# Kernel optimization log

Hardware: AMD Instinct MI355X
Metric: run time of the kernel (lower is better)

The kernel has to match this reference:

```python
import jax, jax.numpy as jnp
import numpy as np

B, WIN, DM, DG, K = 32, 128, 1024, 64, 15  # batch, win_size(node feat dim), d_model(#nodes), graph embed, top_k


def setup_inputs() -> dict:
    key = jax.random.key(0)
    ks = jax.random.split(key, 7)
    sc_in = 1.0 / np.sqrt(WIN)
    return {
        "x": jax.random.normal(ks[0], (B, WIN, DM), jnp.float32),
        "Wq": jax.random.normal(ks[1], (DG, WIN), jnp.float32) * sc_in,
        "bq": jax.random.normal(ks[2], (DG,), jnp.float32) * 0.02,
        "Wk": jax.random.normal(ks[3], (DG, WIN), jnp.float32) * sc_in,
        "bk": jax.random.normal(ks[4], (DG,), jnp.float32) * 0.02,
        "Wg": jax.random.normal(ks[5], (WIN, WIN), jnp.float32) * sc_in,  # GCNConv lin weight [out,in]
        "bg": jax.random.normal(ks[6], (WIN,), jnp.float32) * 0.02,
    }


def _gcn_one(nf, Wq, bq, Wk, bk, Wg, bg):
    # nf: [N, F] node features (N = d_model, F = win_size)
    N = nf.shape[0]
    q = nf @ Wq.T + bq                      # [N, DG]
    k = nf @ Wk.T + bk                      # [N, DG]
    scores = (q @ k.T) * (1.0 / np.sqrt(DG))  # [N, N]
    scores = jnp.where(jnp.eye(N, dtype=bool), -jnp.inf, scores)
    _, tgt = jax.lax.top_k(scores, K)       # [N, K] top-k neighbors per source node
    src = jnp.repeat(jnp.arange(N), K)      # [N*K]
    tgt = tgt.reshape(-1)                   # [N*K]
    loops = jnp.arange(N)
    # manual self loops (module) + self loops added internally by GCNConv (default add_self_loops=True)
    src_all = jnp.concatenate([src, loops, loops])
    tgt_all = jnp.concatenate([tgt, loops, loops])
    # gcn_norm: degree over target (col) with unit edge weights
    deg = jax.ops.segment_sum(jnp.ones_like(tgt_all, jnp.float32), tgt_all, num_segments=N)
    dinv = jnp.where(deg > 0, jax.lax.rsqrt(deg), 0.0)
    norm = dinv[src_all] * dinv[tgt_all]    # [E]
    h = nf @ Wg.T                           # [N, F] linear transform (no bias inside lin)
    msg = h[src_all] * norm[:, None]        # gather + scale
    out = jax.ops.segment_sum(msg, tgt_all, num_segments=N) + bg  # scatter-add + bias
    return out                              # [N, F]


def reference(x, Wq, bq, Wk, bk, Wg, bg):
    # x: [B, win_size, d_model] -> nodes: [B, d_model, win_size]
    nodes = x.transpose(0, 2, 1)
    h = jax.vmap(lambda nf: _gcn_one(nf, Wq, bq, Wk, bk, Wg, bg))(nodes)  # [B, N, F]
    # n_layers == 1: no ReLU/dropout applied after last layer
    return h.transpose(0, 2, 1)  # [B, win_size, d_model]
```

## Files before the change

### kernel.cpp

```cpp
#include <hip/hip_runtime.h>

#define NBATCH 32
#define NN     1024
#define NF     128
#define NDG    64
#define TOPK   15

#define OFF_QH    ((size_t)0)
#define OFF_QL    ((size_t)4194304)
#define OFF_KH    ((size_t)8388608)
#define OFF_KL    ((size_t)12582912)
#define OFF_H     ((size_t)16777216)
#define OFF_DEG   ((size_t)33554432)
#define OFF_BMP   ((size_t)33685504)
#define OFF_WL    ((size_t)37879808)
#define OFF_TOPK  ((size_t)38010880)
#define OFF_W64   ((size_t)40108032)
#define OFF_QT64  ((size_t)40239104)
#define OFF_KT64  ((size_t)57016320)
#define OFF_TMP   ((size_t)0)

typedef short s8v  __attribute__((ext_vector_type(8)));
typedef float f4v  __attribute__((ext_vector_type(4)));
typedef unsigned short us8v __attribute__((ext_vector_type(8)));

__device__ inline unsigned short bf16_rne(float f) {
    unsigned u = __float_as_uint(f);
    return (unsigned short)((u + 0x7FFFu + ((u >> 16) & 1u)) >> 16);
}
__device__ inline float bf16_tof(unsigned short h) { return __uint_as_float(((unsigned)h) << 16); }

__device__ inline unsigned pack22(float s) {
    unsigned u   = __float_as_uint(s);
    int      mag = (int)(u & 0x7FFFFFFFu);
    int      t   = mag - 0x38800000;
    t = t < 0 ? 0 : (t > 0x07FFFFFF ? 0x07FFFFFF : t);
    unsigned ts = (unsigned)t >> 6;
    return ((int)u < 0) ? (0x1FFFFFu - ts) : (0x200000u | ts);
}
__device__ inline float dec22(unsigned val22) {
    bool pos = (val22 & 0x200000u) != 0;
    unsigned ts = pos ? (val22 & 0x1FFFFFu) : (0x1FFFFFu - (val22 & 0x1FFFFFu));
    float f = __uint_as_float((ts << 6) + 0x38800000u);
    return pos ? f : -f;
}

__global__ __launch_bounds__(256) void k_upcast(const float* __restrict__ Wq,
                                                const float* __restrict__ Wk,
                                                double* __restrict__ Wq64,
                                                double* __restrict__ Wk64) {
    int i = blockIdx.x * 256 + threadIdx.x;
    Wq64[i] = (double)Wq[i];
    Wk64[i] = (double)Wk[i];
}

__global__ __launch_bounds__(256) void k_prep(
    const float* __restrict__ x, const float* __restrict__ bq, const float* __restrict__ bk,
    const double* __restrict__ Wq64, const double* __restrict__ Wk64,
    const float* __restrict__ Wg,
    unsigned short* __restrict__ qh, unsigned short* __restrict__ ql,
    unsigned short* __restrict__ kh, unsigned short* __restrict__ kl,
    double* __restrict__ qT64, double* __restrict__ kT64,
    float* __restrict__ h,
    uint4* __restrict__ zbase, int zn)
{
    __shared__ float xs[64 * 129];
    const int t = threadIdx.x;
    const int l = t & 63;
    const int w = t >> 6;
    const int uw = __builtin_amdgcn_readfirstlane(w);
    const int n0 = blockIdx.x * 64;
    const int half = blockIdx.y;
    const int b  = blockIdx.z;

    {
        int lid = ((b * 2 + half) * 16 + blockIdx.x) * 256 + t;
        for (int i = lid; i < zn; i += 262144)
            zbase[i] = make_uint4(0u, 0u, 0u, 0u);
    }

    {
        const int j = t & 63, fg = t >> 6;
        for (int ff = 0; ff < 32; ++ff) {
            int f = fg + ff * 4;
            xs[j * 129 + f] = x[((size_t)b * NF + f) * NN + n0 + j];
        }
    }
    __syncthreads();

    {
        const int d0 = half * 32 + uw * 8;
        double accq[8], acck[8];
        #pragma unroll
        for (int dd = 0; dd < 8; ++dd) {
            accq[dd] = (double)bq[d0 + dd];
            acck[dd] = (double)bk[d0 + dd];
        }
        for (int fc = 0; fc < 32; ++fc) {
            double dx0 = (double)xs[l * 129 + fc * 4 + 0];
            double dx1 = (double)xs[l * 129 + fc * 4 + 1];
            double dx2 = (double)xs[l * 129 + fc * 4 + 2];
            double dx3 = (double)xs[l * 129 + fc * 4 + 3];
            #pragma unroll
            for (int dd = 0; dd < 8; ++dd) {
                int d = d0 + dd;
                const double* wq = &Wq64[d * NF + fc * 4];
                const double* wk = &Wk64[d * NF + fc * 4];
                accq[dd] += dx0 * wq[0] + dx1 * wq[1] + dx2 * wq[2] + dx3 * wq[3];
                acck[dd] += dx0 * wk[0] + dx1 * wk[1] + dx2 * wk[2] + dx3 * wk[3];
            }
        }
        #pragma unroll
        for (int dd = 0; dd < 8; ++dd) {
            size_t idx = ((size_t)b * NDG + d0 + dd) * NN + n0 + l;
            qT64[idx] = accq[dd];
            kT64[idx] = acck[dd];
        }
        us8v qh0, ql0, kh0, kl0;
        #pragma unroll
        for (int dd = 0; dd < 8; ++dd) {
            float fq = (float)accq[dd];
            unsigned short h1 = bf16_rne(fq);
            unsigned short l1 = bf16_rne(fq - bf16_tof(h1));
            float fk = (float)acck[dd];
            unsigned short h2 = bf16_rne(fk);
            unsigned short l2 = bf16_rne(fk - bf16_tof(h2));
            qh0[dd] = h1; ql0[dd] = l1; kh0[dd] = h2; kl0[dd] = l2;
        }
        size_t nb = ((size_t)b * NN + n0 + l) * NDG + d0;
        *(us8v*)&qh[nb] = qh0;
        *(us8v*)&ql[nb] = ql0;
        *(us8v*)&kh[nb] = kh0;
        *(us8v*)&kl[nb] = kl0;
    }

    {
        const int fp0 = half * 64 + uw * 16;
        float acc[16];
        #pragma unroll
        for (int i = 0; i < 16; ++i) acc[i] = 0.f;
        for (int fc = 0; fc < 32; ++fc) {
            float x0 = xs[l * 129 + fc * 4 + 0];
            float x1 = xs[l * 129 + fc * 4 + 1];
            float x2 = xs[l * 129 + fc * 4 + 2];
            float x3 = xs[l * 129 + fc * 4 + 3];
            #pragma unroll
            for (int ff = 0; ff < 16; ++ff) {
                const float* wg = &Wg[(fp0 + ff) * NF + fc * 4];
                acc[ff] += x0 * wg[0] + x1 * wg[1] + x2 * wg[2] + x3 * wg[3];
            }
        }
        __syncthreads();
        #pragma unroll
        for (int ff = 0; ff < 16; ++ff) xs[l * 129 + fp0 + ff] = acc[ff];
        __syncthreads();
        for (int r = 0; r < 16; ++r) {
            int idx = t + 256 * r;
            int n = idx >> 6, f = idx & 63;
            h[((size_t)b * NN + n0 + n) * NF + half * 64 + f] = xs[n * 129 + half * 64 + f];
        }
    }
}

#define CE(x,y) { unsigned a_ = v[x], b_ = v[y]; v[x] = a_ > b_ ? a_ : b_; v[y] = a_ > b_ ? b_ : a_; }
__device__ inline void sort16(unsigned v[16]) {
    CE(0,1) CE(2,3) CE(4,5) CE(6,7) CE(8,9) CE(10,11) CE(12,13) CE(14,15)
    CE(0,2) CE(1,3) CE(4,6) CE(5,7) CE(8,10) CE(9,11) CE(12,14) CE(13,15)
    CE(1,2) CE(5,6) CE(9,10) CE(13,14)
    CE(0,4) CE(1,5) CE(2,6) CE(3,7) CE(8,12) CE(9,13) CE(10,14) CE(11,15)
    CE(2,4) CE(3,5) CE(10,12) CE(11,13)
    CE(1,2) CE(3,4) CE(5,6) CE(9,10) CE(11,12) CE(13,14)
    CE(0,8) CE(1,9) CE(2,10) CE(3,11) CE(4,12) CE(5,13) CE(6,14) CE(7,15)
    CE(4,8) CE(5,9) CE(6,10) CE(7,11)
    CE(2,4) CE(3,5) CE(6,8) CE(7,9) CE(10,12) CE(11,13)
    CE(1,2) CE(3,4) CE(5,6) CE(7,8) CE(9,10) CE(11,12) CE(13,14)
}
__device__ inline void clean16(unsigned v[16]) {
    CE(0,8) CE(1,9) CE(2,10) CE(3,11) CE(4,12) CE(5,13) CE(6,14) CE(7,15)
    CE(0,4) CE(1,5) CE(2,6) CE(3,7) CE(8,12) CE(9,13) CE(10,14) CE(11,15)
    CE(0,2) CE(1,3) CE(4,6) CE(5,7) CE(8,10) CE(9,11) CE(12,14) CE(13,15)
    CE(0,1) CE(2,3) CE(4,5) CE(6,7) CE(8,9) CE(10,11) CE(12,13) CE(14,15)
}

__global__ __launch_bounds__(512, 4) void k_score(
    const unsigned short* __restrict__ qh, const unsigned short* __restrict__ ql,
    const unsigned short* __restrict__ kh, const unsigned short* __restrict__ kl,
    int* __restrict__ deg, unsigned int* __restrict__ bmp,
    int* __restrict__ topk, int* __restrict__ wl_cnt, int* __restrict__ wl)
{
    __shared__ unsigned short pkh[16 * 1024];
    __shared__ unsigned char  pkl[16 * 1024];
    const int t = threadIdx.x, l = t & 63, w = t >> 6;
    const int b = blockIdx.y, row0 = blockIdx.x * 16;
    const int m = l & 15, q4 = l >> 4;

    size_t abase = ((size_t)b * NN + row0 + m) * NDG + q4 * 8;
    s8v ah0 = *(const s8v*)&qh[abase];
    s8v ah1 = *(const s8v*)&qh[abase + 32];
    s8v al0 = *(const s8v*)&ql[abase];
    s8v al1 = *(const s8v*)&ql[abase + 32];

    const int colbase = w * 128;
    #pragma unroll
    for (int tt = 0; tt < 8; ++tt) {
        int col = colbase + tt * 16 + m;
        size_t bbase = ((size_t)b * NN + col) * NDG + q4 * 8;
        s8v bh0 = *(const s8v*)&kh[bbase];
        s8v bh1 = *(const s8v*)&kh[bbase + 32];
        s8v bl0 = *(const s8v*)&kl[bbase];
        s8v bl1 = *(const s8v*)&kl[bbase + 32];
        f4v acc = {0.f, 0.f, 0.f, 0.f};
        acc = __builtin_amdgcn_mfma_f32_16x16x32_bf16(al0, bl0, acc, 0, 0, 0);
        acc = __builtin_amdgcn_mfma_f32_16x16x32_bf16(al1, bl1, acc, 0, 0, 0);
        acc = __builtin_amdgcn_mfma_f32_16x16x32_bf16(ah0, bl0, acc, 0, 0, 0);
        acc = __builtin_amdgcn_mfma_f32_16x16x32_bf16(ah1, bl1, acc, 0, 0, 0);
        acc = __builtin_amdgcn_mfma_f32_16x16x32_bf16(al0, bh0, acc, 0, 0, 0);
        acc = __builtin_amdgcn_mfma_f32_16x16x32_bf16(al1, bh1, acc, 0, 0, 0);
        acc = __builtin_amdgcn_mfma_f32_16x16x32_bf16(ah0, bh0, acc, 0, 0, 0);
        acc = __builtin_amdgcn_mfma_f32_16x16x32_bf16(ah1, bh1, acc, 0, 0, 0);
        #pragma unroll
        for (int r = 0; r < 4; ++r) {
            int row  = q4 * 4 + r;
            int grow = row0 + row;
            float s = acc[r] * 0.125f;
            unsigned c22 = (col == grow) ? 0u : pack22(s);
            int pos = row * 1024 + (col ^ (q4 << 4));
            pkh[pos] = (unsigned short)(c22 >> 6);
            pkl[pos] = (unsigned char)(c22 & 63u);
        }
    }
    __syncthreads();

    for (int rr = 0; rr < 2; ++rr) {
        const int row = 2 * w + rr, grow = row0 + row;
        const int swz = (row >> 2) << 4;
        unsigned v[16];
        #pragma unroll
        for (int j = 0; j < 16; ++j) {
            int idx = row * 1024 + ((l + 64 * j) ^ swz);
            unsigned c22 = ((unsigned)pkh[idx] << 6) | (unsigned)pkl[idx];
            v[j] = (c22 << 10) | (unsigned)(1023 - (l + 64 * j));
        }
        sort16(v);
        #pragma unroll
        for (int off = 1; off < 64; off <<= 1) {
            unsigned pv[16];
            #pragma unroll
            for (int i = 0; i < 16; ++i) pv[i] = (unsigned)__shfl_xor((int)v[i], off, 64);
            #pragma unroll
            for (int i = 0; i < 8; ++i) {
                unsigned a0 = v[i], b0 = pv[15 - i];
                unsigned a1 = v[15 - i], b1 = pv[i];
                v[i]      = a0 > b0 ? a0 : b0;
                v[15 - i] = a1 > b1 ? a1 : b1;
            }
            clean16(v);
        }
        float s15 = dec22(v[14] >> 10), s16 = dec22(v[15] >> 10);
        unsigned e15 = (__float_as_uint(fabsf(s15)) >> 23) & 255u;
        unsigned e16 = (__float_as_uint(fabsf(s16)) >> 23) & 255u;
        unsigned e = e15 > e16 ? e15 : e16;
        float qq = __uint_as_float((e - 17) << 23);
        bool flagged = (s15 - s16) < (4.f * qq + 1e-4f);
        if (l < 15) {
            int col = 1023 - (int)(v[l] & 1023u);
            atomicAdd(&deg[b * NN + col], 1);
            atomicOr(&bmp[((size_t)b * NN + col) * 32 + (grow >> 5)], 1u << (grow & 31));
            if (flagged) topk[(b * NN + grow) * 16 + l] = col;
        }
        if (l == 0 && flagged) {
            int idx = atomicAdd(wl_cnt, 1);
            if (idx < 32767) wl[idx] = b * NN + grow;
        }
    }
}

__global__ __launch_bounds__(64) void k_repair(
    const double* __restrict__ qT64, const double* __restrict__ kT64,
    const int* __restrict__ topk, const int* __restrict__ wl_cnt, const int* __restrict__ wl,
    int* __restrict__ deg, unsigned int* __restrict__ bmp)
{
    const int l = threadIdx.x;
    __shared__ double qld[64];
    __shared__ int oldset[15], newset[15];
    const double NEGINF = -__builtin_inf();
    int n = wl_cnt[0]; if (n > 32767) n = 32767;

    for (int i = blockIdx.x; i < n; i += 1024) {
        int rg = wl[i];
        int b = rg >> 10, row = rg & 1023;

        __syncthreads();
        qld[l] = qT64[((size_t)b * NDG + l) * NN + row];
        if (l < 15) oldset[l] = topk[(b * NN + row) * 16 + l];
        __syncthreads();

        double sc[16];
        #pragma unroll
        for (int tt = 0; tt < 16; ++tt) sc[tt] = 0.0;
        const double* kb = &kT64[(size_t)b * NDG * NN];
        double buf[16];
        #pragma unroll
        for (int tt = 0; tt < 16; ++tt) buf[tt] = kb[l + 64 * tt];
        for (int d = 0; d < 64; ++d) {
            double nb[16];
            if (d < 63) {
                const double* kr = kb + (size_t)(d + 1) * NN;
                #pragma unroll
                for (int tt = 0; tt < 16; ++tt) nb[tt] = kr[l + 64 * tt];
            }
            double qd = qld[d];
            #pragma unroll
            for (int tt = 0; tt < 16; ++tt) sc[tt] += qd * buf[tt];
            if (d < 63) {
                #pragma unroll
                for (int tt = 0; tt < 16; ++tt) buf[tt] = nb[tt];
            }
        }
        #pragma unroll
        for (int tt = 0; tt < 16; ++tt) if (l + 64 * tt == row) sc[tt] = NEGINF;

        for (int it = 0; it < 15; ++it) {
            double lv = NEGINF; int lc = 0x7fffffff;
            #pragma unroll
            for (int tt = 0; tt < 16; ++tt)
                if (sc[tt] > lv) { lv = sc[tt]; lc = l + 64 * tt; }
            #pragma unroll
            for (int off = 1; off < 64; off <<= 1) {
                double ov = __shfl_xor(lv, off, 64);
                int    oc = __shfl_xor(lc, off, 64);
                if (ov > lv || (ov == lv && oc < lc)) { lv = ov; lc = oc; }
            }
            #pragma unroll
            for (int tt = 0; tt < 16; ++tt) if (l + 64 * tt == lc) sc[tt] = NEGINF;
            if (l == 0) newset[it] = lc;
        }
        __syncthreads();
        if (l < 15) {
            int cn = newset[l];
            bool found = false;
            #pragma unroll
            for (int j = 0; j < 15; ++j) found = found || (oldset[j] == cn);
            if (!found) {
                atomicAdd(&deg[b * NN + cn], 1);
                atomicOr(&bmp[((size_t)b * NN + cn) * 32 + (row >> 5)], 1u << (row & 31));
            }
            int co = oldset[l];
            found = false;
            #pragma unroll
            for (int j = 0; j < 15; ++j) found = found || (newset[j] == co);
            if (!found) {
                atomicSub(&deg[b * NN + co], 1);
                atomicAnd(&bmp[((size_t)b * NN + co) * 32 + (row >> 5)], ~(1u << (row & 31)));
            }
        }
    }
}

__global__ __launch_bounds__(128) void k_gather(
    const float* __restrict__ h, const float* __restrict__ bg,
    const int* __restrict__ deg, const unsigned int* __restrict__ bmp,
    float* __restrict__ tmp)
{
    __shared__ int list[1024];
    __shared__ float nrm[1024];
    __shared__ int scnt;
    const int tgt = blockIdx.x, b = blockIdx.y, t = threadIdx.x;
    if (t < 32) {
        unsigned word = bmp[((size_t)b * NN + tgt) * 32 + t];
        int pc = __popc(word);
        int pre = pc;
        #pragma unroll
        for (int d = 1; d < 32; d <<= 1) {
            int o = __shfl_up(pre, d, 32);
            if (t >= d) pre += o;
        }
        if (t == 31) scnt = pre;
        int idx = pre - pc;
        while (word) {
            int s = __ffs(word) - 1;
            word &= word - 1;
            list[idx++] = t * 32 + s;
        }
    }
    __syncthreads();
    const int cnt = scnt;
    for (int e = t; e < cnt; e += 128)
        nrm[e] = rsqrtf((float)(deg[b * NN + list[e]] + 2));
    __syncthreads();
    const int f = t;
    float dt = rsqrtf((float)(deg[b * NN + tgt] + 2));
    float acc = 2.0f * dt * h[((size_t)b * NN + tgt) * NF + f];
    for (int e = 0; e < cnt; ++e) {
        int src = list[e];
        acc += h[((size_t)b * NN + src) * NF + f] * nrm[e];
    }
    tmp[((size_t)b * NN + tgt) * NF + f] = bg[f] + dt * acc;
}

__global__ __launch_bounds__(256) void k_transpose(const float* __restrict__ tmp,
                                                   float* __restrict__ out)
{
    __shared__ float tile[32][33];
    const int t = threadIdx.x;
    const int n0 = blockIdx.x * 32, f0 = blockIdx.y * 32, b = blockIdx.z;
    const int c = t & 31, rb = t >> 5;
    #pragma unroll
    for (int i = 0; i < 4; ++i) {
        int r = rb + i * 8;
        tile[r][c] = tmp[((size_t)b * NN + n0 + r) * NF + f0 + c];
    }
    __syncthreads();
    #pragma unroll
    for (int i = 0; i < 4; ++i) {
        int r = rb + i * 8;
        out[((size_t)b * NF + f0 + r) * NN + n0 + c] = tile[c][r];
    }
}

extern "C" void kernel_launch(void* const* d_in, const int* in_sizes, int n_in,
                              void* d_out, int out_size, void* d_ws, size_t ws_size,
                              hipStream_t stream)
{
    const float* x  = (const float*)d_in[0];
    const float* Wq = (const float*)d_in[1];
    const float* bq = (const float*)d_in[2];
    const float* Wk = (const float*)d_in[3];
    const float* bk = (const float*)d_in[4];
    const float* Wg = (const float*)d_in[5];
    const float* bg = (const float*)d_in[6];
    float* out = (float*)d_out;
    char* ws = (char*)d_ws;

    unsigned short* qh = (unsigned short*)(ws + OFF_QH);
    unsigned short* ql = (unsigned short*)(ws + OFF_QL);
    unsigned short* kh = (unsigned short*)(ws + OFF_KH);
    unsigned short* kl = (unsigned short*)(ws + OFF_KL);
    float*          h   = (float*)(ws + OFF_H);
    int*            deg = (int*)(ws + OFF_DEG);
    unsigned int*   bmp = (unsigned int*)(ws + OFF_BMP);
    int*            wlc = (int*)(ws + OFF_WL);
    int*            wl  = wlc + 1;
    int*            tpk = (int*)(ws + OFF_TOPK);
    double*         Wq64 = (double*)(ws + OFF_W64);
    double*         Wk64 = Wq64 + 8192;
    double*         qT64 = (double*)(ws + OFF_QT64);
    double*         kT64 = (double*)(ws + OFF_KT64);
    float*          tmp  = (float*)(ws + OFF_TMP);

    k_upcast<<<32, 256, 0, stream>>>(Wq, Wk, Wq64, Wk64);
    k_prep<<<dim3(16, 2, 32), 256, 0, stream>>>(x, bq, bk, Wq64, Wk64, Wg,
                                                qh, ql, kh, kl, qT64, kT64, h,
                                                (uint4*)(ws + OFF_DEG), 270337);
    k_score<<<dim3(64, 32), 512, 0, stream>>>(qh, ql, kh, kl, deg, bmp, tpk, wlc, wl);
    k_repair<<<1024, 64, 0, stream>>>(qT64, kT64, tpk, wlc, wl, deg, bmp);
    k_gather<<<dim3(1024, 32), 128, 0, stream>>>(h, bg, deg, bmp, tmp);
    k_transpose<<<dim3(32, 4, 32), 256, 0, stream>>>(tmp, out);
}
```

Before: 311.6 us.

## Replace full wave bitonic top-k with threshold-filtered candidate selection

Each lane now takes the max of its 16 scores, and a 64-wide bitonic sort of those maxes gives the 16th-largest lane max as a threshold. Only elements at or above the threshold are compacted through shared memory and sorted once with a single 64-element bitonic sort. The full 1024-element merge sort stays as a fallback when more than 64 candidates survive. Scores are now stored as one packed 32-bit key (score plus column) instead of split short and byte arrays. This grows shared memory from 48KB to 64KB per block, which may lower occupancy.

```diff
diff --git a/kernel.cpp b/kernel.cpp
--- a/kernel.cpp
+++ b/kernel.cpp
@@ -182,14 +182,28 @@
     CE(0,1) CE(2,3) CE(4,5) CE(6,7) CE(8,9) CE(10,11) CE(12,13) CE(14,15)
 }
 
+__device__ inline unsigned bsort64(unsigned v, int l) {
+    #pragma unroll
+    for (int k = 2; k <= 64; k <<= 1) {
+        #pragma unroll
+        for (int j = k >> 1; j >= 1; j >>= 1) {
+            unsigned pv = (unsigned)__shfl_xor((int)v, j, 64);
+            bool tm = ((l & k) == 0) == ((l & j) == 0);
+            unsigned hi = v > pv ? v : pv;
+            unsigned lo = v > pv ? pv : v;
+            v = tm ? hi : lo;
+        }
+    }
+    return v;
+}
+
 __global__ __launch_bounds__(512, 4) void k_score(
     const unsigned short* __restrict__ qh, const unsigned short* __restrict__ ql,
     const unsigned short* __restrict__ kh, const unsigned short* __restrict__ kl,
     int* __restrict__ deg, unsigned int* __restrict__ bmp,
     int* __restrict__ topk, int* __restrict__ wl_cnt, int* __restrict__ wl)
 {
-    __shared__ unsigned short pkh[16 * 1024];
-    __shared__ unsigned char  pkl[16 * 1024];
+    __shared__ unsigned pk[16 * 1024];
     const int t = threadIdx.x, l = t & 63, w = t >> 6;
     const int b = blockIdx.y, row0 = blockIdx.x * 16;
     const int m = l & 15, q4 = l >> 4;
@@ -224,46 +238,77 @@
             int grow = row0 + row;
             float s = acc[r] * 0.125f;
             unsigned c22 = (col == grow) ? 0u : pack22(s);
-            int pos = row * 1024 + (col ^ (q4 << 4));
-            pkh[pos] = (unsigned short)(c22 >> 6);
-            pkl[pos] = (unsigned char)(c22 & 63u);
+            pk[row * 1024 + (col ^ (q4 << 4))] = (c22 << 10) | (unsigned)(1023 - col);
         }
     }
     __syncthreads();
 
     for (int rr = 0; rr < 2; ++rr) {
         const int row = 2 * w + rr, grow = row0 + row;
-        const int swz = (row >> 2) << 4;
         unsigned v[16];
         #pragma unroll
-        for (int j = 0; j < 16; ++j) {
-            int idx = row * 1024 + ((l + 64 * j) ^ swz);
-            unsigned c22 = ((unsigned)pkh[idx] << 6) | (unsigned)pkl[idx];
-            v[j] = (c22 << 10) | (unsigned)(1023 - (l + 64 * j));
-        }
-        sort16(v);
-        #pragma unroll
-        for (int off = 1; off < 64; off <<= 1) {
-            unsigned pv[16];
-            #pragma unroll
-            for (int i = 0; i < 16; ++i) pv[i] = (unsigned)__shfl_xor((int)v[i], off, 64);
-            #pragma unroll
-            for (int i = 0; i < 8; ++i) {
-                unsigned a0 = v[i], b0 = pv[15 - i];
-                unsigned a1 = v[15 - i], b1 = pv[i];
-                v[i]      = a0 > b0 ? a0 : b0;
-                v[15 - i] = a1 > b1 ? a1 : b1;
-            }
-            clean16(v);
-        }
-        float s15 = dec22(v[14] >> 10), s16 = dec22(v[15] >> 10);
+        for (int j = 0; j < 16; ++j)
+            v[j] = pk[row * 1024 + l + 64 * j];
+
+        unsigned lmax = v[0];
+        #pragma unroll
+        for (int j = 1; j < 16; ++j) lmax = v[j] > lmax ? v[j] : lmax;
+
+        unsigned sm = bsort64(lmax, l);
+        unsigned T = (unsigned)__shfl((int)sm, 15, 64);
+
+        int cnt = 0;
+        #pragma unroll
+        for (int j = 0; j < 16; ++j) cnt += (v[j] >= T) ? 1 : 0;
+        int pre = cnt;
+        #pragma unroll
+        for (int d = 1; d < 64; d <<= 1) {
+            int o = __shfl_up(pre, d, 64);
+            if (l >= d) pre += o;
+        }
+        const int C = __shfl(pre, 63, 64);
+        int off = pre - cnt;
+
+        unsigned res;
+        if (C <= 64) {
+            unsigned* scr = &pk[row * 1024];
+            #pragma unroll
+            for (int j = 0; j < 16; ++j)
+                if (v[j] >= T) scr[off++] = v[j];
+            unsigned cv = (l < C) ? scr[l] : 0u;
+            res = bsort64(cv, l);
+        } else {
+            sort16(v);
+            #pragma unroll
+            for (int offb = 1; offb < 64; offb <<= 1) {
+                unsigned pv[16];
+                #pragma unroll
+                for (int i = 0; i < 16; ++i) pv[i] = (unsigned)__shfl_xor((int)v[i], offb, 64);
+                #pragma unroll
+                for (int i = 0; i < 8; ++i) {
+                    unsigned a0 = v[i], b0 = pv[15 - i];
+                    unsigned a1 = v[15 - i], b1 = pv[i];
+                    v[i]      = a0 > b0 ? a0 : b0;
+                    v[15 - i] = a1 > b1 ? a1 : b1;
+                }
+                clean16(v);
+            }
+            unsigned rsel = v[15];
+            #pragma unroll
+            for (int j = 0; j < 15; ++j) if (l == j) rsel = v[j];
+            res = rsel;
+        }
+
+        unsigned r14 = (unsigned)__shfl((int)res, 14, 64);
+        unsigned r15 = (unsigned)__shfl((int)res, 15, 64);
+        float s15 = dec22(r14 >> 10), s16 = dec22(r15 >> 10);
         unsigned e15 = (__float_as_uint(fabsf(s15)) >> 23) & 255u;
         unsigned e16 = (__float_as_uint(fabsf(s16)) >> 23) & 255u;
         unsigned e = e15 > e16 ? e15 : e16;
         float qq = __uint_as_float((e - 17) << 23);
         bool flagged = (s15 - s16) < (4.f * qq + 1e-4f);
         if (l < 15) {
-            int col = 1023 - (int)(v[l] & 1023u);
+            int col = 1023 - (int)(res & 1023u);
             atomicAdd(&deg[b * NN + col], 1);
             atomicOr(&bmp[((size_t)b * NN + col) * 32 + (grow >> 5)], 1u << (grow & 31));
             if (flagged) topk[(b * NN + grow) * 16 + l] = col;
```

After: 317.0 us. No clear change (+1.7%).
